# Performance work log

Hardware: AMD Instinct MI355X
Metric: run time of the kernel (lower is better)

## Reference

```python
import jax, jax.numpy as jnp
import numpy as np

FP8_E4M3_MAX = 448.0
F32_TINY = np.float32(np.finfo(np.float32).tiny)


def setup_inputs() -> dict:
    key = jax.random.key(0)
    k1, k2, k3, k4 = jax.random.split(key, 4)
    B, S, D_IN, D_OUT, BLK = 4, 2048, 4096, 4096, 128
    x = jax.random.normal(k1, (B, S, D_IN), dtype=jnp.float32)
    # Simulated fp8 weight values (post-quantization codes stored as f32) and
    # per-(row, in-block) scales, as produced by a blockwise weight quantizer.
    weight_fp8 = jax.random.normal(k2, (D_OUT, D_IN), dtype=jnp.float32)
    weight_scale = jax.random.uniform(k3, (D_OUT, D_IN // BLK), dtype=jnp.float32, minval=1e-3, maxval=1.0)
    bias = jax.random.normal(k4, (D_OUT,), dtype=jnp.float32)
    return {"x": x, "weight_fp8": weight_fp8, "weight_scale": weight_scale, "bias": bias, "blk": BLK}


def reference(x, weight_fp8, weight_scale, bias, blk):
    orig_dtype = x.dtype
    x32 = x.astype(jnp.float32)
    *batch_dims, last = x32.shape
    leading = int(np.prod(batch_dims)) if batch_dims else 1
    nblk = last // blk
    blocks = x32.reshape(leading, nblk, blk)             # [T, nblk, blk]
    amax = jnp.max(jnp.abs(blocks), axis=-1)             # [T, nblk]
    x_scales = jnp.maximum(amax / FP8_E4M3_MAX, F32_TINY)
    # pow2 rounding of activation scales (use_activation_pow2_scale=True)
    x_scales = jnp.exp2(jnp.round(jnp.log2(jnp.maximum(x_scales, F32_TINY))))
    s = x_scales[..., None]
    x_dq = ((blocks / s) * s).reshape(leading, last)     # quantize-emulate then dequant
    # weight dequant: bf16 scale broadcast over in-dim blocks
    w_scale = weight_scale.astype(jnp.bfloat16).astype(jnp.float32)  # [O, nblk]
    w_dq = (weight_fp8.reshape(weight_fp8.shape[0], nblk, blk) * w_scale[:, :, None]).reshape(weight_fp8.shape)
    y = x_dq @ w_dq.T + bias[None, :]                    # [T, O]
    return y.reshape(*batch_dims, -1).astype(orig_dtype)
```

## Files before the change

kernel.cpp:

```cpp
#include <hip/hip_runtime.h>
#include <cstdint>
#include <cstddef>


typedef __attribute__((ext_vector_type(8))) __bf16 bf16x8;
typedef __attribute__((ext_vector_type(4))) float f32x4;

__device__ __forceinline__ unsigned short bf16rn(float f) {
  unsigned u = __builtin_bit_cast(unsigned, f);
  u = (u + 0x7FFFu + ((u >> 16) & 1u)) >> 16;
  return (unsigned short)u;
}
__device__ __forceinline__ float bf16tof(unsigned short h) {
  unsigned u = ((unsigned)h) << 16;
  return __builtin_bit_cast(float, u);
}
__device__ __forceinline__ void gload_lds16(const void* g, void* l) {
  __builtin_amdgcn_global_load_lds(
      (const __attribute__((address_space(1))) unsigned int*)g,
      (__attribute__((address_space(3))) unsigned int*)l, 16, 0, 0);
}


__global__ __launch_bounds__(256) void k_convert_x(
    const float* __restrict__ x, unsigned short* __restrict__ xb, int n8) {
  int t = blockIdx.x * 256 + threadIdx.x;
  if (t >= n8) return;
  const float4* p = (const float4*)x + (size_t)t * 2;
  float4 a = p[0], b = p[1];
  uint4 o;
  o.x = (unsigned)bf16rn(a.x) | ((unsigned)bf16rn(a.y) << 16);
  o.y = (unsigned)bf16rn(a.z) | ((unsigned)bf16rn(a.w) << 16);
  o.z = (unsigned)bf16rn(b.x) | ((unsigned)bf16rn(b.y) << 16);
  o.w = (unsigned)bf16rn(b.z) | ((unsigned)bf16rn(b.w) << 16);
  ((uint4*)xb)[t] = o;
}

__global__ __launch_bounds__(256) void k_dequant_w(
    const float* __restrict__ w, const float* __restrict__ sc,
    unsigned short* __restrict__ wb, int K, int nblk, int blk, int n8) {
  int t = blockIdx.x * 256 + threadIdx.x;
  if (t >= n8) return;
  size_t base = (size_t)t * 8;
  int o_row = (int)(base / (size_t)K);
  int k = (int)(base % (size_t)K);
  float s = bf16tof(bf16rn(sc[(size_t)o_row * nblk + k / blk]));
  const float4* p = (const float4*)w + (size_t)t * 2;
  float4 a = p[0], b = p[1];
  uint4 o;
  o.x = (unsigned)bf16rn(a.x * s) | ((unsigned)bf16rn(a.y * s) << 16);
  o.y = (unsigned)bf16rn(a.z * s) | ((unsigned)bf16rn(a.w * s) << 16);
  o.z = (unsigned)bf16rn(b.x * s) | ((unsigned)bf16rn(b.y * s) << 16);
  o.w = (unsigned)bf16rn(b.z * s) | ((unsigned)bf16rn(b.w * s) << 16);
  ((uint4*)wb)[t] = o;
}


#define BM 256
#define BN 256
#define BK 64

#define BAR() __builtin_amdgcn_s_barrier()
#define WAIT_LGKM0() asm volatile("s_waitcnt lgkmcnt(0)" ::: "memory")
#define WAIT_VM(n) asm volatile("s_waitcnt vmcnt(" #n ")" ::: "memory")
#define SCHEDB() __builtin_amdgcn_sched_barrier(0)
#define PRIO(p) __builtin_amdgcn_s_setprio(p)

#define STG_A(buf, q, tile)                                               \
  gload_lds16(Ag + (size_t)(q) * 64 * Ks + (size_t)(tile) * BK,           \
              smem + (buf) * 65536 + (q) * 8192 + tid16)
#define STG_B(buf, q, tile)                                               \
  gload_lds16(Bg + (size_t)(q) * 64 * Ks + (size_t)(tile) * BK,           \
              smem + (buf) * 65536 + 32768 + (q) * 8192 + tid16)

#define READ_A(arr, buf, qm)                                              \
  _Pragma("unroll") for (int i_ = 0; i_ < 4; ++i_) {                      \
    arr[i_][0] = *(const bf16x8*)(smem + (buf) * 65536 +                  \
        (wr * 128 + (qm) * 64 + i_ * 16 + lr) * 128 + ko0);               \
    arr[i_][1] = *(const bf16x8*)(smem + (buf) * 65536 +                  \
        (wr * 128 + (qm) * 64 + i_ * 16 + lr) * 128 + ko1);               \
  }
#define READ_B(arr, buf, qn)                                              \
  _Pragma("unroll") for (int j_ = 0; j_ < 2; ++j_) {                      \
    arr[j_][0] = *(const bf16x8*)(smem + (buf) * 65536 + 32768 +          \
        (wc * 64 + (qn) * 32 + j_ * 16 + lr) * 128 + ko0);                \
    arr[j_][1] = *(const bf16x8*)(smem + (buf) * 65536 + 32768 +          \
        (wc * 64 + (qn) * 32 + j_ * 16 + lr) * 128 + ko1);                \
  }
#define MFMA_Q(qm, qn, aarr, barr)                                        \
  _Pragma("unroll") for (int kk_ = 0; kk_ < 2; ++kk_)                     \
  _Pragma("unroll") for (int i_ = 0; i_ < 4; ++i_)                        \
  _Pragma("unroll") for (int j_ = 0; j_ < 2; ++j_)                        \
    acc[(qm) * 4 + i_][(qn) * 2 + j_] =                                   \
        __builtin_amdgcn_mfma_f32_16x16x32_bf16(                          \
            aarr[i_][kk_], barr[j_][kk_],                                 \
            acc[(qm) * 4 + i_][(qn) * 2 + j_], 0, 0, 0);

__global__ __launch_bounds__(512, 2) void k_gemm256(
    const unsigned short* __restrict__ A, const unsigned short* __restrict__ B,
    const float* __restrict__ bias, float* __restrict__ C,
    int M, int N, int K) {
  extern __shared__ __align__(16) char smem[];

  const int nbn = N / BN;
  const int nwg = gridDim.x;
  int bid = blockIdx.x;
  int wg = bid;
  if ((nwg & 7) == 0) wg = (bid & 7) * (nwg >> 3) + (bid >> 3);
  const int m0 = (wg / nbn) * BM;
  const int n0 = (wg % nbn) * BN;

  const int tid = threadIdx.x;
  const int lane = tid & 63;
  const int wid = tid >> 6;
  const int wr = wid >> 2;
  const int wc = wid & 3;
  const int lr = lane & 15;
  const int ko0 = (((lane >> 4) * 16) ^ ((lane & 7) << 4));
  const int ko1 = ((64 | ((lane >> 4) * 16)) ^ ((lane & 7) << 4));
  const int tid16 = tid * 16;

  const int srow = tid >> 3;
  const int sgran = (tid & 7) ^ (srow & 7);
  const size_t Ks = (size_t)K;
  const unsigned short* Ag = A + (size_t)(m0 + srow) * Ks + sgran * 8;
  const unsigned short* Bg = B + (size_t)(n0 + srow) * Ks + sgran * 8;

  f32x4 acc[8][4] = {};
  bf16x8 a0[4][2], a1[4][2], b0[2][2], b1[2][2];

  const int NT = K / BK;
  const int NITER = NT / 2;

  STG_A(0, 0, 0); STG_A(0, 2, 0); STG_B(0, 0, 0); STG_B(0, 1, 0);
  STG_A(0, 1, 0); STG_A(0, 3, 0); STG_B(0, 2, 0); STG_B(0, 3, 0);
  STG_A(1, 0, 1); STG_A(1, 2, 1); STG_B(1, 0, 1); STG_B(1, 1, 1);
  STG_A(1, 1, 1); STG_A(1, 3, 1);
  WAIT_VM(6);
  BAR();

  for (int it = 0; it < NITER; ++it) {
    const int t = 2 * it;
    const bool s2 = (t + 2) < NT;
    const bool s3 = (t + 3) < NT;
    SCHEDB();
    READ_A(a0, 0, 0); READ_B(b0, 0, 0);
    STG_B(1, 2, t + 1); STG_B(1, 3, t + 1);
    SCHEDB(); BAR(); WAIT_LGKM0(); SCHEDB();
    PRIO(1); MFMA_Q(0, 0, a0, b0); PRIO(0); SCHEDB(); BAR();
    SCHEDB();
    READ_B(b1, 0, 1);
    if (s2) { STG_A(0, 0, t + 2); STG_A(0, 2, t + 2); }
    SCHEDB(); BAR(); WAIT_LGKM0(); SCHEDB();
    PRIO(1); MFMA_Q(0, 1, a0, b1); PRIO(0); SCHEDB(); BAR();
    SCHEDB();
    READ_A(a1, 0, 1);
    if (s2) { STG_B(0, 0, t + 2); STG_B(0, 1, t + 2); }
    SCHEDB(); BAR(); WAIT_LGKM0(); SCHEDB();
    PRIO(1); MFMA_Q(1, 0, a1, b0); PRIO(0); SCHEDB(); BAR();
    SCHEDB();
    if (s2) { STG_A(0, 1, t + 2); STG_A(0, 3, t + 2); WAIT_VM(6); }
    else    { WAIT_VM(0); }
    BAR(); SCHEDB();
    PRIO(1); MFMA_Q(1, 1, a1, b1); PRIO(0); SCHEDB(); BAR();
    SCHEDB();
    READ_A(a0, 1, 0); READ_B(b0, 1, 0);
    if (s2) { STG_B(0, 2, t + 2); STG_B(0, 3, t + 2); }
    SCHEDB(); BAR(); WAIT_LGKM0(); SCHEDB();
    PRIO(1); MFMA_Q(0, 0, a0, b0); PRIO(0); SCHEDB(); BAR();
    SCHEDB();
    READ_B(b1, 1, 1);
    if (s3) { STG_A(1, 0, t + 3); STG_A(1, 2, t + 3); }
    SCHEDB(); BAR(); WAIT_LGKM0(); SCHEDB();
    PRIO(1); MFMA_Q(0, 1, a0, b1); PRIO(0); SCHEDB(); BAR();
    SCHEDB();
    READ_A(a1, 1, 1);
    if (s3) { STG_B(1, 0, t + 3); STG_B(1, 1, t + 3); }
    SCHEDB(); BAR(); WAIT_LGKM0(); SCHEDB();
    PRIO(1); MFMA_Q(1, 0, a1, b0); PRIO(0); SCHEDB(); BAR();
    SCHEDB();
    if (s3)      { STG_A(1, 1, t + 3); STG_A(1, 3, t + 3); WAIT_VM(6); }
    else if (s2) { WAIT_VM(0); }
    BAR(); SCHEDB();
    PRIO(1); MFMA_Q(1, 1, a1, b1); PRIO(0); SCHEDB(); BAR();
  }

  const int col0 = n0 + wc * 64 + (lane & 15);
  const int row0 = m0 + wr * 128 + ((lane >> 4) << 2);
#pragma unroll
  for (int j = 0; j < 4; ++j) {
    float bj = bias[col0 + j * 16];
#pragma unroll
    for (int i = 0; i < 8; ++i) {
#pragma unroll
      for (int r = 0; r < 4; ++r) {
        C[(size_t)(row0 + i * 16 + r) * N + (col0 + j * 16)] = acc[i][j][r] + bj;
      }
    }
  }
}


__global__ __launch_bounds__(256) void k_fallback(
    const float* __restrict__ x, const float* __restrict__ w,
    const float* __restrict__ sc, const float* __restrict__ bias,
    float* __restrict__ out, int T, int O, int K, int nblk, int blk) {
  long long idx = (long long)blockIdx.x * 256 + threadIdx.x;
  if (idx >= (long long)T * O) return;
  int row = (int)(idx / O), col = (int)(idx % O);
  const float* xr = x + (size_t)row * K;
  const float* wr = w + (size_t)col * K;
  const float* sr = sc + (size_t)col * nblk;
  float acc = 0.f;
  for (int b = 0; b < nblk; ++b) {
    float s = bf16tof(bf16rn(sr[b]));
    float part = 0.f;
    for (int k = 0; k < blk; k += 4) {
      float4 xa = *(const float4*)(xr + b * blk + k);
      float4 wa = *(const float4*)(wr + b * blk + k);
      part += xa.x * wa.x + xa.y * wa.y + xa.z * wa.z + xa.w * wa.w;
    }
    acc += part * s;
  }
  out[idx] = acc + bias[col];
}

extern "C" void kernel_launch(void* const* d_in, const int* in_sizes, int n_in,
                              void* d_out, int out_size, void* d_ws, size_t ws_size,
                              hipStream_t stream) {
  const float* x = (const float*)d_in[0];
  const float* w = (const float*)d_in[1];
  const float* sc = (const float*)d_in[2];
  const float* bias = (const float*)d_in[3];
  float* out = (float*)d_out;

  const int x_n = in_sizes[0];
  const int w_n = in_sizes[1];
  const int s_n = in_sizes[2];
  const int O = in_sizes[3];
  const int K = w_n / O;
  const int T = x_n / K;
  const int nblk = s_n / O;
  const int blk = K / nblk;

  const size_t need = (size_t)x_n * 2 + (size_t)w_n * 2;
  const bool tiled_ok = ws_size >= need && (K % (2 * BK)) == 0 &&
                        (T % BM) == 0 && (O % BN) == 0 && (blk % 8) == 0 &&
                        K >= 2 * BK;

  if (tiled_ok) {
    unsigned short* xb = (unsigned short*)d_ws;
    unsigned short* wb = xb + (size_t)x_n;
    int n8x = x_n / 8, n8w = w_n / 8;
    k_convert_x<<<(n8x + 255) / 256, 256, 0, stream>>>(x, xb, n8x);
    k_dequant_w<<<(n8w + 255) / 256, 256, 0, stream>>>(w, sc, wb, K, nblk, blk, n8w);
    hipFuncSetAttribute((const void*)k_gemm256,
                        hipFuncAttributeMaxDynamicSharedMemorySize, 131072);
    dim3 grid((T / BM) * (O / BN));
    k_gemm256<<<grid, 512, 131072, stream>>>(xb, wb, bias, out, T, O, K);
  } else {
    long long total = (long long)T * O;
    dim3 grid((unsigned)((total + 255) / 256));
    k_fallback<<<grid, 256, 0, stream>>>(x, w, sc, bias, out, T, O, K, nblk, blk);
  }
}
```

Baseline: 293.5 us.

## Merge prep kernels and software-pipeline LDS reads with MFMA in GEMM loop

```diff
diff --git a/kernel.cpp b/kernel.cpp
--- a/kernel.cpp
+++ b/kernel.cpp
@@ -22,37 +22,36 @@
 }
 
 
-__global__ __launch_bounds__(256) void k_convert_x(
-    const float* __restrict__ x, unsigned short* __restrict__ xb, int n8) {
+__global__ __launch_bounds__(256) void k_prep(
+    const float* __restrict__ x, const float* __restrict__ w,
+    const float* __restrict__ sc, unsigned short* __restrict__ xb,
+    unsigned short* __restrict__ wb, int K, int nblk, int blk,
+    int n8x, int n8w) {
   int t = blockIdx.x * 256 + threadIdx.x;
-  if (t >= n8) return;
-  const float4* p = (const float4*)x + (size_t)t * 2;
-  float4 a = p[0], b = p[1];
-  uint4 o;
-  o.x = (unsigned)bf16rn(a.x) | ((unsigned)bf16rn(a.y) << 16);
-  o.y = (unsigned)bf16rn(a.z) | ((unsigned)bf16rn(a.w) << 16);
-  o.z = (unsigned)bf16rn(b.x) | ((unsigned)bf16rn(b.y) << 16);
-  o.w = (unsigned)bf16rn(b.z) | ((unsigned)bf16rn(b.w) << 16);
-  ((uint4*)xb)[t] = o;
-}
-
-__global__ __launch_bounds__(256) void k_dequant_w(
-    const float* __restrict__ w, const float* __restrict__ sc,
-    unsigned short* __restrict__ wb, int K, int nblk, int blk, int n8) {
-  int t = blockIdx.x * 256 + threadIdx.x;
-  if (t >= n8) return;
-  size_t base = (size_t)t * 8;
-  int o_row = (int)(base / (size_t)K);
-  int k = (int)(base % (size_t)K);
-  float s = bf16tof(bf16rn(sc[(size_t)o_row * nblk + k / blk]));
-  const float4* p = (const float4*)w + (size_t)t * 2;
-  float4 a = p[0], b = p[1];
-  uint4 o;
-  o.x = (unsigned)bf16rn(a.x * s) | ((unsigned)bf16rn(a.y * s) << 16);
-  o.y = (unsigned)bf16rn(a.z * s) | ((unsigned)bf16rn(a.w * s) << 16);
-  o.z = (unsigned)bf16rn(b.x * s) | ((unsigned)bf16rn(b.y * s) << 16);
-  o.w = (unsigned)bf16rn(b.z * s) | ((unsigned)bf16rn(b.w * s) << 16);
-  ((uint4*)wb)[t] = o;
+  if (t < n8x) {
+    const float4* p = (const float4*)x + (size_t)t * 2;
+    float4 a = p[0], b = p[1];
+    uint4 o;
+    o.x = (unsigned)bf16rn(a.x) | ((unsigned)bf16rn(a.y) << 16);
+    o.y = (unsigned)bf16rn(a.z) | ((unsigned)bf16rn(a.w) << 16);
+    o.z = (unsigned)bf16rn(b.x) | ((unsigned)bf16rn(b.y) << 16);
+    o.w = (unsigned)bf16rn(b.z) | ((unsigned)bf16rn(b.w) << 16);
+    ((uint4*)xb)[t] = o;
+  } else if (t - n8x < n8w) {
+    int tw = t - n8x;
+    size_t base = (size_t)tw * 8;
+    int o_row = (int)(base / (size_t)K);
+    int k = (int)(base % (size_t)K);
+    float s = bf16tof(bf16rn(sc[(size_t)o_row * nblk + k / blk]));
+    const float4* p = (const float4*)w + (size_t)tw * 2;
+    float4 a = p[0], b = p[1];
+    uint4 o;
+    o.x = (unsigned)bf16rn(a.x * s) | ((unsigned)bf16rn(a.y * s) << 16);
+    o.y = (unsigned)bf16rn(a.z * s) | ((unsigned)bf16rn(a.w * s) << 16);
+    o.z = (unsigned)bf16rn(b.x * s) | ((unsigned)bf16rn(b.y * s) << 16);
+    o.w = (unsigned)bf16rn(b.z * s) | ((unsigned)bf16rn(b.w * s) << 16);
+    ((uint4*)wb)[tw] = o;
+  }
 }
 
 
@@ -61,7 +60,6 @@
 #define BK 64
 
 #define BAR() __builtin_amdgcn_s_barrier()
-#define WAIT_LGKM0() asm volatile("s_waitcnt lgkmcnt(0)" ::: "memory")
 #define WAIT_VM(n) asm volatile("s_waitcnt vmcnt(" #n ")" ::: "memory")
 #define SCHEDB() __builtin_amdgcn_sched_barrier(0)
 #define PRIO(p) __builtin_amdgcn_s_setprio(p)
@@ -135,54 +133,67 @@
   STG_A(0, 0, 0); STG_A(0, 2, 0); STG_B(0, 0, 0); STG_B(0, 1, 0);
   STG_A(0, 1, 0); STG_A(0, 3, 0); STG_B(0, 2, 0); STG_B(0, 3, 0);
   STG_A(1, 0, 1); STG_A(1, 2, 1); STG_B(1, 0, 1); STG_B(1, 1, 1);
-  STG_A(1, 1, 1); STG_A(1, 3, 1);
-  WAIT_VM(6);
-  BAR();
+  STG_A(1, 1, 1); STG_A(1, 3, 1); STG_B(1, 2, 1); STG_B(1, 3, 1);
+  WAIT_VM(8);
+  BAR(); SCHEDB();
+  READ_A(a0, 0, 0); READ_B(b0, 0, 0);
 
   for (int it = 0; it < NITER; ++it) {
     const int t = 2 * it;
-    const bool s2 = (t + 2) < NT;
-    const bool s3 = (t + 3) < NT;
-    SCHEDB();
-    READ_A(a0, 0, 0); READ_B(b0, 0, 0);
-    STG_B(1, 2, t + 1); STG_B(1, 3, t + 1);
-    SCHEDB(); BAR(); WAIT_LGKM0(); SCHEDB();
-    PRIO(1); MFMA_Q(0, 0, a0, b0); PRIO(0); SCHEDB(); BAR();
-    SCHEDB();
+    const bool pf = (t + 2) < NT;
+    PRIO(1);
     READ_B(b1, 0, 1);
-    if (s2) { STG_A(0, 0, t + 2); STG_A(0, 2, t + 2); }
-    SCHEDB(); BAR(); WAIT_LGKM0(); SCHEDB();
-    PRIO(1); MFMA_Q(0, 1, a0, b1); PRIO(0); SCHEDB(); BAR();
-    SCHEDB();
+    MFMA_Q(0, 0, a0, b0);
+    PRIO(0); BAR();
+    if (pf) { STG_A(0, 0, t + 2); STG_A(0, 2, t + 2); }
+    PRIO(1);
     READ_A(a1, 0, 1);
-    if (s2) { STG_B(0, 0, t + 2); STG_B(0, 1, t + 2); }
-    SCHEDB(); BAR(); WAIT_LGKM0(); SCHEDB();
-    PRIO(1); MFMA_Q(1, 0, a1, b0); PRIO(0); SCHEDB(); BAR();
-    SCHEDB();
-    if (s2) { STG_A(0, 1, t + 2); STG_A(0, 3, t + 2); WAIT_VM(6); }
-    else    { WAIT_VM(0); }
+    MFMA_Q(0, 1, a0, b1);
+    PRIO(0); BAR();
+    if (pf) { STG_B(0, 0, t + 2); STG_B(0, 1, t + 2); }
+    PRIO(1);
+    MFMA_Q(1, 0, a1, b0);
+    PRIO(0); BAR();
+    if (pf) {
+      STG_A(0, 1, t + 2); STG_A(0, 3, t + 2);
+      STG_B(0, 2, t + 2); STG_B(0, 3, t + 2);
+      WAIT_VM(8);
+    } else {
+      WAIT_VM(0);
+    }
     BAR(); SCHEDB();
-    PRIO(1); MFMA_Q(1, 1, a1, b1); PRIO(0); SCHEDB(); BAR();
-    SCHEDB();
+    PRIO(1);
     READ_A(a0, 1, 0); READ_B(b0, 1, 0);
-    if (s2) { STG_B(0, 2, t + 2); STG_B(0, 3, t + 2); }
-    SCHEDB(); BAR(); WAIT_LGKM0(); SCHEDB();
-    PRIO(1); MFMA_Q(0, 0, a0, b0); PRIO(0); SCHEDB(); BAR();
-    SCHEDB();
+    MFMA_Q(1, 1, a1, b1);
+    PRIO(0); BAR();
+    PRIO(1);
     READ_B(b1, 1, 1);
-    if (s3) { STG_A(1, 0, t + 3); STG_A(1, 2, t + 3); }
-    SCHEDB(); BAR(); WAIT_LGKM0(); SCHEDB();
-    PRIO(1); MFMA_Q(0, 1, a0, b1); PRIO(0); SCHEDB(); BAR();
-    SCHEDB();
+    MFMA_Q(0, 0, a0, b0);
+    PRIO(0); BAR();
+    if (pf) { STG_A(1, 0, t + 3); STG_A(1, 2, t + 3); }
+    PRIO(1);
     READ_A(a1, 1, 1);
-    if (s3) { STG_B(1, 0, t + 3); STG_B(1, 1, t + 3); }
-    SCHEDB(); BAR(); WAIT_LGKM0(); SCHEDB();
-    PRIO(1); MFMA_Q(1, 0, a1, b0); PRIO(0); SCHEDB(); BAR();
-    SCHEDB();
-    if (s3)      { STG_A(1, 1, t + 3); STG_A(1, 3, t + 3); WAIT_VM(6); }
-    else if (s2) { WAIT_VM(0); }
-    BAR(); SCHEDB();
-    PRIO(1); MFMA_Q(1, 1, a1, b1); PRIO(0); SCHEDB(); BAR();
+    MFMA_Q(0, 1, a0, b1);
+    PRIO(0); BAR();
+    if (pf) { STG_B(1, 0, t + 3); STG_B(1, 1, t + 3); }
+    PRIO(1);
+    MFMA_Q(1, 0, a1, b0);
+    PRIO(0); BAR();
+    if (pf) {
+      STG_A(1, 1, t + 3); STG_A(1, 3, t + 3);
+      STG_B(1, 2, t + 3); STG_B(1, 3, t + 3);
+      WAIT_VM(8);
+      BAR(); SCHEDB();
+      PRIO(1);
+      READ_A(a0, 0, 0); READ_B(b0, 0, 0);
+      MFMA_Q(1, 1, a1, b1);
+      PRIO(0); BAR();
+    } else {
+      BAR();
+      PRIO(1);
+      MFMA_Q(1, 1, a1, b1);
+      PRIO(0);
+    }
   }
 
   const int col0 = n0 + wc * 64 + (lane & 15);
@@ -252,8 +263,9 @@
     unsigned short* xb = (unsigned short*)d_ws;
     unsigned short* wb = xb + (size_t)x_n;
     int n8x = x_n / 8, n8w = w_n / 8;
-    k_convert_x<<<(n8x + 255) / 256, 256, 0, stream>>>(x, xb, n8x);
-    k_dequant_w<<<(n8w + 255) / 256, 256, 0, stream>>>(w, sc, wb, K, nblk, blk, n8w);
+    int nprep = n8x + n8w;
+    k_prep<<<(nprep + 255) / 256, 256, 0, stream>>>(x, w, sc, xb, wb, K, nblk,
+                                                    blk, n8x, n8w);
     hipFuncSetAttribute((const void*)k_gemm256,
                         hipFuncAttributeMaxDynamicSharedMemorySize, 131072);
     dim3 grid((T / BM) * (O / BN));
```

Result: slower. 843.8 us (+187.5%).
